# Optimization experiments

Measured on AMD Instinct MI355X. Metric: run time of the kernel, lower is better.

Reference implementation:

```python
import jax, jax.numpy as jnp
import numpy as np

T, B, D_IN, NQ = 256, 2048, 128, 8  # time, batch, input_dim, n_qubits == hidden_dim


def setup_inputs() -> dict:
    key = jax.random.key(0)
    ks = jax.random.split(key, 13)
    s = 1.0 / np.sqrt(D_IN + NQ)
    def lin(ka, kb):
        W = jax.random.uniform(ka, (D_IN + NQ, NQ), jnp.float32, -s, s)
        b = jax.random.uniform(kb, (NQ,), jnp.float32, -s, s)
        return W, b
    Wf, bf = lin(ks[0], ks[1])
    Wi, bi = lin(ks[2], ks[3])
    Wg, bg = lin(ks[4], ks[5])
    Wo, bo = lin(ks[6], ks[7])
    # trainable RX angles per wire for each of the 4 quantum gates
    thf = jax.random.normal(ks[8], (NQ,), jnp.float32) * 0.1
    thi = jax.random.normal(ks[9], (NQ,), jnp.float32) * 0.1
    thg = jax.random.normal(ks[10], (NQ,), jnp.float32) * 0.1
    tho = jax.random.normal(ks[11], (NQ,), jnp.float32) * 0.1
    inputs = jax.random.normal(ks[12], (T, B, D_IN), jnp.float32)
    return {"inputs": inputs, "Wf": Wf, "bf": bf, "Wi": Wi, "bi": bi,
            "Wg": Wg, "bg": bg, "Wo": Wo, "bo": bo,
            "thf": thf, "thi": thi, "thg": thg, "tho": tho}


def _qgate(lin_out, theta):
    # |0..0> -> RX(x_i) encode -> RX(theta_i) trainable -> <PauliZ_i> = cos(x_i + theta_i)
    return jnp.cos(lin_out + theta)


def reference(inputs, Wf, bf, Wi, bi, Wg, bg, Wo, bo, thf, thi, thg, tho):
    Bsz = inputs.shape[1]
    h0 = jnp.zeros((Bsz, NQ), inputs.dtype)
    c0 = jnp.zeros((Bsz, NQ), inputs.dtype)

    def step(carry, x):
        hx, cx = carry
        comb = jnp.concatenate([x, hx], axis=1)  # [B, D_IN+NQ]
        f = jax.nn.sigmoid(_qgate(comb @ Wf + bf, thf))
        i = jax.nn.sigmoid(_qgate(comb @ Wi + bi, thi))
        g = jnp.tanh(_qgate(comb @ Wg + bg, thg))
        o = jax.nn.sigmoid(_qgate(comb @ Wo + bo, tho))
        cx = f * cx + i * g
        hx = o * jnp.tanh(cx)
        return (hx, cx), hx

    (hx, cx), outputs = jax.lax.scan(step, (h0, c0), inputs)
    return outputs, hx, cx
```

## Files before the change

### kernel.cpp

```cpp
#include <hip/hip_runtime.h>

#define T_DIM 256
#define B_DIM 2048
#define D_IN_DIM 128
#define NQ 8
#define ROWS_PER_BLK 128
#define TSTRIDE 33

#define XSIDX(row, k) (((row) << 7) + ((k) ^ ((row) & 31)))

__global__ __launch_bounds__(256) void qlstm_gemm(
    const float* __restrict__ X,
    const float* __restrict__ Wf, const float* __restrict__ Wi,
    const float* __restrict__ Wg, const float* __restrict__ Wo,
    const float* __restrict__ bf, const float* __restrict__ bi,
    const float* __restrict__ bg, const float* __restrict__ bo,
    const float* __restrict__ thf, const float* __restrict__ thi,
    const float* __restrict__ thg, const float* __restrict__ tho,
    float4* __restrict__ Z)
{
    __shared__ float xs[ROWS_PER_BLK * D_IN_DIM];

    const int t = (int)threadIdx.x;
    const int r0 = (int)blockIdx.x * ROWS_PER_BLK;

    const float4* Xg = (const float4*)(X + (size_t)r0 * D_IN_DIM);
#pragma unroll
    for (int i = 0; i < 16; i++) {
        int L = t + i * 256;
        float4 v = Xg[L];
        int row = L >> 5;
        int k0  = (L & 31) * 4;
        xs[XSIDX(row, k0 + 0)] = v.x;
        xs[XSIDX(row, k0 + 1)] = v.y;
        xs[XSIDX(row, k0 + 2)] = v.z;
        xs[XSIDX(row, k0 + 3)] = v.w;
    }
    __syncthreads();

    const int wid  = __builtin_amdgcn_readfirstlane(t >> 6);
    const int lane = t & 63;

    const float* W  = (wid == 0) ? Wf  : (wid == 1) ? Wi  : (wid == 2) ? Wg  : Wo;
    const float* BB = (wid == 0) ? bf  : (wid == 1) ? bi  : (wid == 2) ? bg  : bo;
    const float* TH = (wid == 0) ? thf : (wid == 1) ? thi : (wid == 2) ? thg : tho;
    const float4* __restrict__ W4 = (const float4*)W;

    float acc0[NQ], acc1[NQ];
#pragma unroll
    for (int q = 0; q < NQ; q++) { float b0 = BB[q] + TH[q]; acc0[q] = b0; acc1[q] = b0; }

    const float* xr0 = &xs[(size_t)lane << 7];
    const float* xr1 = &xs[(size_t)(lane + 64) << 7];
    const int sw = lane & 31;
#pragma unroll 4
    for (int k = 0; k < D_IN_DIM; k++) {
        float x0 = xr0[k ^ sw];
        float x1 = xr1[k ^ sw];
        float4 wa = W4[2 * k];
        float4 wb = W4[2 * k + 1];
        acc0[0] += x0 * wa.x; acc0[1] += x0 * wa.y; acc0[2] += x0 * wa.z; acc0[3] += x0 * wa.w;
        acc0[4] += x0 * wb.x; acc0[5] += x0 * wb.y; acc0[6] += x0 * wb.z; acc0[7] += x0 * wb.w;
        acc1[0] += x1 * wa.x; acc1[1] += x1 * wa.y; acc1[2] += x1 * wa.z; acc1[3] += x1 * wa.w;
        acc1[4] += x1 * wb.x; acc1[5] += x1 * wb.y; acc1[6] += x1 * wb.z; acc1[7] += x1 * wb.w;
    }

    __syncthreads();
    float* tile = xs;
#pragma unroll
    for (int q = 0; q < NQ; q++) {
        tile[lane * TSTRIDE + q * 4 + wid] = acc0[q];
        tile[(lane + 64) * TSTRIDE + q * 4 + wid] = acc1[q];
    }
    __syncthreads();

    float4* Zblk = Z + (size_t)r0 * NQ;
#pragma unroll
    for (int i = 0; i < 4; i++) {
        int F = t + i * 256;
        int r = F >> 3, q = F & 7;
        const float* s = &tile[r * TSTRIDE + q * 4];
        Zblk[F] = make_float4(s[0], s[1], s[2], s[3]);
    }
}

#define INV_2PI 0.15915494309189535f
#define L2E     1.4426950408889634f

__device__ __forceinline__ float hw_cos(float x) {
    return __builtin_amdgcn_cosf(x * INV_2PI);
}
__device__ __forceinline__ float hw_sig(float x) {
    return __builtin_amdgcn_rcpf(1.0f + __builtin_amdgcn_exp2f(-L2E * x));
}
__device__ __forceinline__ float hw_tanh(float x) {
    return 1.0f - 2.0f * __builtin_amdgcn_rcpf(__builtin_amdgcn_exp2f((2.0f * L2E) * x) + 1.0f);
}

#define BCAST8(x, J) \
    __int_as_float(__builtin_amdgcn_ds_swizzle(__float_as_int(x), ((J) << 5) | 0x18))

#define LSTM_STEP_R(zv, hdst) { \
    float h0 = BCAST8(h, 0), h1 = BCAST8(h, 1), h2 = BCAST8(h, 2), h3 = BCAST8(h, 3); \
    float h4 = BCAST8(h, 4), h5 = BCAST8(h, 5), h6 = BCAST8(h, 6), h7 = BCAST8(h, 7); \
    float f0 = fmaf(h0, whf[0], (zv).x), f1 = fmaf(h1, whf[1], 0.0f); \
    float i0 = fmaf(h0, whi[0], (zv).y), i1 = fmaf(h1, whi[1], 0.0f); \
    float g0 = fmaf(h0, whg[0], (zv).z), g1 = fmaf(h1, whg[1], 0.0f); \
    float o0 = fmaf(h0, who[0], (zv).w), o1 = fmaf(h1, who[1], 0.0f); \
    f0 = fmaf(h2, whf[2], f0); f1 = fmaf(h3, whf[3], f1); \
    i0 = fmaf(h2, whi[2], i0); i1 = fmaf(h3, whi[3], i1); \
    g0 = fmaf(h2, whg[2], g0); g1 = fmaf(h3, whg[3], g1); \
    o0 = fmaf(h2, who[2], o0); o1 = fmaf(h3, who[3], o1); \
    f0 = fmaf(h4, whf[4], f0); f1 = fmaf(h5, whf[5], f1); \
    i0 = fmaf(h4, whi[4], i0); i1 = fmaf(h5, whi[5], i1); \
    g0 = fmaf(h4, whg[4], g0); g1 = fmaf(h5, whg[5], g1); \
    o0 = fmaf(h4, who[4], o0); o1 = fmaf(h5, who[5], o1); \
    f0 = fmaf(h6, whf[6], f0); f1 = fmaf(h7, whf[7], f1); \
    i0 = fmaf(h6, whi[6], i0); i1 = fmaf(h7, whi[7], i1); \
    g0 = fmaf(h6, whg[6], g0); g1 = fmaf(h7, whg[7], g1); \
    o0 = fmaf(h6, who[6], o0); o1 = fmaf(h7, who[7], o1); \
    float fg = hw_sig(hw_cos(f0 + f1)); \
    float ig = hw_sig(hw_cos(i0 + i1)); \
    float gg = hw_tanh(hw_cos(g0 + g1)); \
    float og = hw_sig(hw_cos(o0 + o1)); \
    c = fmaf(fg, c, ig * gg); \
    h = og * hw_tanh(c); \
    (hdst) = h; }

__global__ __launch_bounds__(64) void qlstm_recur(
    const float4* __restrict__ Z,
    const float* __restrict__ Wf, const float* __restrict__ Wi,
    const float* __restrict__ Wg, const float* __restrict__ Wo,
    float* __restrict__ out,
    float* __restrict__ state,
    int t0, int ct, int first, int last)
{
    const int tid = (int)blockIdx.x * 64 + (int)threadIdx.x;
    const int q   = tid & 7;

    float whf[8], whi[8], whg[8], who[8];
#pragma unroll
    for (int j = 0; j < 8; j++) {
        whf[j] = Wf[(D_IN_DIM + j) * NQ + q];
        whi[j] = Wi[(D_IN_DIM + j) * NQ + q];
        whg[j] = Wg[(D_IN_DIM + j) * NQ + q];
        who[j] = Wo[(D_IN_DIM + j) * NQ + q];
    }

    float h, c;
    if (first) { h = 0.0f; c = 0.0f; }
    else       { h = state[tid]; c = state[B_DIM * NQ + tid]; }

    const size_t stepsz = (size_t)B_DIM * NQ;
    const float4* Zp = Z + tid;
    float* og_ptr = out + (size_t)t0 * stepsz + tid;

    float4 bufA[8], bufB[8];
    float houtA[8], houtB[8];
#pragma unroll
    for (int s = 0; s < 8; s++) bufA[s] = Zp[(size_t)s * stepsz];

    for (int tb = 0; tb < ct; tb += 16) {
#pragma unroll
        for (int s = 0; s < 8; s++) bufB[s] = Zp[(size_t)(tb + 8 + s) * stepsz];
        __builtin_amdgcn_sched_barrier(0);
#pragma unroll
        for (int s = 0; s < 8; s++) {
            float4 z = bufA[s];
            LSTM_STEP_R(z, houtA[s])
        }
        if (tb + 16 < ct) {
#pragma unroll
            for (int s = 0; s < 8; s++) bufA[s] = Zp[(size_t)(tb + 16 + s) * stepsz];
        }
        __builtin_amdgcn_sched_barrier(0);
#pragma unroll
        for (int s = 0; s < 8; s++) og_ptr[(size_t)s * stepsz] = houtA[s];
#pragma unroll
        for (int s = 0; s < 8; s++) {
            float4 z = bufB[s];
            LSTM_STEP_R(z, houtB[s])
        }
#pragma unroll
        for (int s = 0; s < 8; s++) og_ptr[(size_t)(8 + s) * stepsz] = houtB[s];
        og_ptr += (size_t)16 * stepsz;
    }

    if (last) {
        out[(size_t)T_DIM * stepsz + tid] = h;
        out[(size_t)T_DIM * stepsz + stepsz + tid] = c;
    } else {
        state[tid] = h;
        state[B_DIM * NQ + tid] = c;
    }
}

extern "C" void kernel_launch(void* const* d_in, const int* in_sizes, int n_in,
                              void* d_out, int out_size, void* d_ws, size_t ws_size,
                              hipStream_t stream) {
    const float* X   = (const float*)d_in[0];
    const float* Wf  = (const float*)d_in[1];
    const float* bf  = (const float*)d_in[2];
    const float* Wi  = (const float*)d_in[3];
    const float* bi  = (const float*)d_in[4];
    const float* Wg  = (const float*)d_in[5];
    const float* bg  = (const float*)d_in[6];
    const float* Wo  = (const float*)d_in[7];
    const float* bo  = (const float*)d_in[8];
    const float* thf = (const float*)d_in[9];
    const float* thi = (const float*)d_in[10];
    const float* thg = (const float*)d_in[11];
    const float* tho = (const float*)d_in[12];
    float* out = (float*)d_out;

    const size_t state_bytes = (size_t)2 * B_DIM * NQ * sizeof(float);
    float* state = (float*)d_ws;
    float4* Zbuf = (float4*)((char*)d_ws + state_bytes);
    size_t avail = ws_size > state_bytes ? ws_size - state_bytes : 0;
    const size_t z_bytes_per_t = (size_t)B_DIM * NQ * sizeof(float4);
    int maxChunkT = (int)(avail / z_bytes_per_t);
    if (maxChunkT > T_DIM) maxChunkT = T_DIM;
    maxChunkT &= ~15;
    if (maxChunkT < 16) maxChunkT = 16;

    int t0 = 0;
    int first = 1;
    while (t0 < T_DIM) {
        int ct = (T_DIM - t0 < maxChunkT) ? (T_DIM - t0) : maxChunkT;
        int rows = ct * B_DIM;
        qlstm_gemm<<<rows / ROWS_PER_BLK, 256, 0, stream>>>(
            X + (size_t)t0 * B_DIM * D_IN_DIM,
            Wf, Wi, Wg, Wo, bf, bi, bg, bo, thf, thi, thg, tho,
            Zbuf);
        int last = (t0 + ct == T_DIM) ? 1 : 0;
        qlstm_recur<<<(B_DIM * NQ) / 64, 64, 0, stream>>>(
            Zbuf, Wf, Wi, Wg, Wo, out, state, t0, ct, first, last);
        t0 += ct;
        first = 0;
    }
}
```

Before: 479.8 us.

## Halve rows per GEMM block, stage weights in LDS, pad x tile

```diff
diff --git a/kernel.cpp b/kernel.cpp
--- a/kernel.cpp
+++ b/kernel.cpp
@@ -4,10 +4,9 @@
 #define B_DIM 2048
 #define D_IN_DIM 128
 #define NQ 8
-#define ROWS_PER_BLK 128
+#define ROWS_PER_BLK 64
+#define XSTRIDE 129
 #define TSTRIDE 33
-
-#define XSIDX(row, k) (((row) << 7) + ((k) ^ ((row) & 31)))
 
 __global__ __launch_bounds__(256) void qlstm_gemm(
     const float* __restrict__ X,
@@ -19,64 +18,63 @@
     const float* __restrict__ thg, const float* __restrict__ tho,
     float4* __restrict__ Z)
 {
-    __shared__ float xs[ROWS_PER_BLK * D_IN_DIM];
+    __shared__ float xs[ROWS_PER_BLK * XSTRIDE];
+    __shared__ float wsh[4 * D_IN_DIM * NQ];
 
     const int t = (int)threadIdx.x;
     const int r0 = (int)blockIdx.x * ROWS_PER_BLK;
 
+    const int wid  = __builtin_amdgcn_readfirstlane(t >> 6);
+    const int lane = t & 63;
+
+    const float* W  = (wid == 0) ? Wf  : (wid == 1) ? Wi  : (wid == 2) ? Wg  : Wo;
+    const float* BB = (wid == 0) ? bf  : (wid == 1) ? bi  : (wid == 2) ? bg  : bo;
+    const float* TH = (wid == 0) ? thf : (wid == 1) ? thi : (wid == 2) ? thg : tho;
+
+    {
+        const float4* Wg4 = (const float4*)W;
+        float4* wd = (float4*)&wsh[wid * (D_IN_DIM * NQ)];
+#pragma unroll
+        for (int j = 0; j < 4; j++) wd[j * 64 + lane] = Wg4[j * 64 + lane];
+    }
+
     const float4* Xg = (const float4*)(X + (size_t)r0 * D_IN_DIM);
 #pragma unroll
-    for (int i = 0; i < 16; i++) {
+    for (int i = 0; i < 8; i++) {
         int L = t + i * 256;
         float4 v = Xg[L];
         int row = L >> 5;
-        int k0  = (L & 31) * 4;
-        xs[XSIDX(row, k0 + 0)] = v.x;
-        xs[XSIDX(row, k0 + 1)] = v.y;
-        xs[XSIDX(row, k0 + 2)] = v.z;
-        xs[XSIDX(row, k0 + 3)] = v.w;
+        int k4  = L & 31;
+        float* d = &xs[row * XSTRIDE + k4 * 4];
+        d[0] = v.x; d[1] = v.y; d[2] = v.z; d[3] = v.w;
     }
     __syncthreads();
 
-    const int wid  = __builtin_amdgcn_readfirstlane(t >> 6);
-    const int lane = t & 63;
-
-    const float* W  = (wid == 0) ? Wf  : (wid == 1) ? Wi  : (wid == 2) ? Wg  : Wo;
-    const float* BB = (wid == 0) ? bf  : (wid == 1) ? bi  : (wid == 2) ? bg  : bo;
-    const float* TH = (wid == 0) ? thf : (wid == 1) ? thi : (wid == 2) ? thg : tho;
-    const float4* __restrict__ W4 = (const float4*)W;
-
-    float acc0[NQ], acc1[NQ];
-#pragma unroll
-    for (int q = 0; q < NQ; q++) { float b0 = BB[q] + TH[q]; acc0[q] = b0; acc1[q] = b0; }
-
-    const float* xr0 = &xs[(size_t)lane << 7];
-    const float* xr1 = &xs[(size_t)(lane + 64) << 7];
-    const int sw = lane & 31;
+    float acc[NQ];
+#pragma unroll
+    for (int q = 0; q < NQ; q++) acc[q] = BB[q] + TH[q];
+
+    const float*  xrow = &xs[lane * XSTRIDE];
+    const float4* wk   = (const float4*)&wsh[wid * (D_IN_DIM * NQ)];
 #pragma unroll 4
     for (int k = 0; k < D_IN_DIM; k++) {
-        float x0 = xr0[k ^ sw];
-        float x1 = xr1[k ^ sw];
-        float4 wa = W4[2 * k];
-        float4 wb = W4[2 * k + 1];
-        acc0[0] += x0 * wa.x; acc0[1] += x0 * wa.y; acc0[2] += x0 * wa.z; acc0[3] += x0 * wa.w;
-        acc0[4] += x0 * wb.x; acc0[5] += x0 * wb.y; acc0[6] += x0 * wb.z; acc0[7] += x0 * wb.w;
-        acc1[0] += x1 * wa.x; acc1[1] += x1 * wa.y; acc1[2] += x1 * wa.z; acc1[3] += x1 * wa.w;
-        acc1[4] += x1 * wb.x; acc1[5] += x1 * wb.y; acc1[6] += x1 * wb.z; acc1[7] += x1 * wb.w;
+        float xk = xrow[k];
+        float4 wa = wk[2 * k];
+        float4 wb = wk[2 * k + 1];
+        acc[0] += xk * wa.x; acc[1] += xk * wa.y; acc[2] += xk * wa.z; acc[3] += xk * wa.w;
+        acc[4] += xk * wb.x; acc[5] += xk * wb.y; acc[6] += xk * wb.z; acc[7] += xk * wb.w;
     }
 
     __syncthreads();
     float* tile = xs;
 #pragma unroll
-    for (int q = 0; q < NQ; q++) {
-        tile[lane * TSTRIDE + q * 4 + wid] = acc0[q];
-        tile[(lane + 64) * TSTRIDE + q * 4 + wid] = acc1[q];
-    }
+    for (int q = 0; q < NQ; q++)
+        tile[lane * TSTRIDE + q * 4 + wid] = acc[q];
     __syncthreads();
 
     float4* Zblk = Z + (size_t)r0 * NQ;
 #pragma unroll
-    for (int i = 0; i < 4; i++) {
+    for (int i = 0; i < 2; i++) {
         int F = t + i * 256;
         int r = F >> 3, q = F & 7;
         const float* s = &tile[r * TSTRIDE + q * 4];
```

Result: faster. 443.7 us (-7.5%).
